# Optimization experiments

Hardware: AMD Instinct MI355X
Metric: run time of the kernel (lower is better)

Reference implementation:

```python
import jax, jax.numpy as jnp
import numpy as np

WS = 7        # window_size
HEADS = 8     # n_heads
SHIFT = WS // 2  # roll amount when shifted=True


def setup_inputs() -> dict:
    key = jax.random.key(0)
    k1, k2, k3 = jax.random.split(key, 3)
    B, C, H, W = 4, 256, 224, 224
    x = jax.random.normal(k1, (B, C, H, W), dtype=jnp.float32)
    # 1x1 conv weight [3C, C] (kernel dims squeezed) and bias [3C]
    w_qkv = jax.random.normal(k2, (3 * C, C), dtype=jnp.float32) * (1.0 / np.sqrt(C))
    b_qkv = jax.random.normal(k3, (3 * C,), dtype=jnp.float32) * 0.02
    return {"x": x, "w_qkv": w_qkv, "b_qkv": b_qkv}


def reference(x, w_qkv, b_qkv):
    B, C, H, W = x.shape
    hd = C // HEADS                      # head dim
    Hn, Wn = H // WS, W // WS            # windows per side

    # shifted: roll spatial dims by -window_size//2
    xs = jnp.roll(x, (-SHIFT, -SHIFT), axis=(-2, -1))

    # 1x1 conv: [B,C,H,W] -> [B,3C,H,W]
    qkv = jnp.einsum('bchw,oc->bohw', xs, w_qkv) + b_qkv[None, :, None, None]

    # window partition: [B,3C,H,W] -> (3, B, Hn, Wn, heads, ws*ws, hd)
    w = qkv.reshape(B, 3, HEADS, hd, Hn, WS, Wn, WS)
    w = jnp.transpose(w, (1, 0, 4, 6, 2, 5, 7, 3))  # 3,B,Hn,Wn,heads,ws,ws,hd
    w = w.reshape(3, B, Hn, Wn, HEADS, WS * WS, hd)
    q, k, v = w[0], w[1], w[2]

    # per-window SDPA (torch default scale = 1/sqrt(head_dim), no mask)
    scale = 1.0 / np.sqrt(hd)
    scores = jnp.einsum('bxyhqd,bxyhkd->bxyhqk', q, k) * scale
    attn = jax.nn.softmax(scores, axis=-1)
    out = jnp.einsum('bxyhqk,bxyhkd->bxyhqd', attn, v)  # B,Hn,Wn,heads,ws2,hd

    # window merge: back to [B,C,H,W]
    out = out.reshape(B, Hn, Wn, HEADS, WS, WS, hd)
    out = jnp.transpose(out, (0, 3, 6, 1, 4, 2, 5))  # B,heads,hd,Hn,ws,Wn,ws
    out = out.reshape(B, C, H, W)

    # inverse roll
    out = jnp.roll(out, (SHIFT, SHIFT), axis=(-2, -1))
    return out
```

## Files before the change

### kernel.cpp

```cpp
#include <hip/hip_runtime.h>

typedef __attribute__((ext_vector_type(8))) __bf16 bf16x8;
typedef __attribute__((ext_vector_type(4))) __bf16 bf16x4;
typedef __attribute__((ext_vector_type(4))) float f32x4;

#define MFMA16(a, b, c) __builtin_amdgcn_mfma_f32_16x16x32_bf16(a, b, c, 0, 0, 0)

#define BAR() asm volatile("s_waitcnt lgkmcnt(0)\n\ts_barrier" ::: "memory")

constexpr int HH = 224, WW = 224, CC = 256;
constexpr int HW = HH * WW;
constexpr int SH = 3;
constexpr int NTOK = 49;

constexpr int QS = 40;
constexpr int VTS = 68;
constexpr int PS = 72;
constexpr int XSS = 264;
constexpr int SZ_QK = 2 * NTOK * QS;
constexpr int OFF_VT = SZ_QK;
constexpr int SZ_VT = 32 * VTS;
constexpr int XS_OFF = OFF_VT + SZ_VT;
constexpr int SMEM_SZ = XS_OFF + NTOK * XSS;

__global__ void __launch_bounds__(256) cvt_w(const float* __restrict__ w,
                                             __bf16* __restrict__ o) {
  int i = blockIdx.x * 256 + threadIdx.x;
  int e = i & 7;
  int l15 = (i >> 3) & 15;
  int quad = (i >> 7) & 3;
  int ks = (i >> 9) & 7;
  int g = i >> 12;
  int h = g / 6, nip = g - h * 6;
  int row = (nip >> 1) * 256 + h * 32 + (nip & 1) * 16 + l15;
  int col = ks * 32 + quad * 8 + e;
  o[i] = (__bf16)w[row * 256 + col];
}

__global__ void __launch_bounds__(256, 4)
swin_attn(const float* __restrict__ x, const __bf16* __restrict__ wbf,
          const float* __restrict__ bias, float* __restrict__ out) {
  __shared__ __bf16 sm[SMEM_SZ];

  const int tid = threadIdx.x;
  const int lane = tid & 63;
  const int wave = tid >> 6;
  const int quad = lane >> 4;
  const int l15 = lane & 15;
  const int wa = wave >> 1, wb = wave & 1;

  int blk = blockIdx.x;
  int win = (blk & 7) * 512 + (blk >> 3);
  int b = win >> 10;
  int hn = (win >> 5) & 31;
  int wn = win & 31;
  int r0 = hn * 7, c0 = wn * 7;

  for (int idx = tid; idx < NTOK * CC; idx += 256) {
    int c = idx / NTOK;
    int p = idx - c * NTOK;
    int pi = p / 7, pj = p - pi * 7;
    int gr = r0 + pi + SH; if (gr >= HH) gr -= HH;
    int gc = c0 + pj + SH; if (gc >= WW) gc -= WW;
    sm[XS_OFF + p * XSS + c] = (__bf16)x[((b * CC + c) * HH + gr) * WW + gc];
  }

  int stok = wave * 16 + l15;
  bool svalid = stok < NTOK;
  int spix;
  {
    int t = svalid ? stok : 48;
    int pi = t / 7, pj = t - pi * 7;
    int gr = r0 + pi + SH; if (gr >= HH) gr -= HH;
    int gc = c0 + pj + SH; if (gc >= WW) gc -= WW;
    spix = gr * WW + gc;
  }

  __bf16* qq = sm;
  __bf16* kk = sm + NTOK * QS;
  __bf16* vT = sm + OFF_VT;
  __bf16* P = sm;
  const float scale = 0.17677669529663687f;
  const f32x4 zero = {0.f, 0.f, 0.f, 0.f};

  const __bf16* wlane = wbf + quad * 128 + l15 * 8;

  for (int h = 0; h < 8; h++) {
    BAR();

    float bs[3];
    f32x4 acc[2][3];
#pragma unroll
    for (int i = 0; i < 3; i++) {
      int nip = 3 * wb + i;
      int o = (nip >> 1) * 256 + h * 32 + (nip & 1) * 16 + l15;
      bs[i] = bias[o];
      acc[0][i] = zero;
      acc[1][i] = zero;
    }
    const __bf16* wp = wlane + (h * 6 + 3 * wb) * 4096;

    bf16x8 wfr[4][3];
#pragma unroll
    for (int pk = 0; pk < 4; pk++)
#pragma unroll
      for (int i = 0; i < 3; i++)
        wfr[pk][i] = *(const bf16x8*)(wp + i * 4096 + pk * 512);

#pragma unroll
    for (int ks = 0; ks < 8; ks++) {
      bf16x8 bfr[3], afr[2];
#pragma unroll
      for (int i = 0; i < 3; i++) bfr[i] = wfr[ks & 3][i];
      if (ks < 4) {
#pragma unroll
        for (int i = 0; i < 3; i++)
          wfr[ks & 3][i] = *(const bf16x8*)(wp + i * 4096 + (ks + 4) * 512);
      }
#pragma unroll
      for (int mil = 0; mil < 2; mil++) {
        int m = (2 * wa + mil) * 16 + l15; if (m > 48) m = 48;
        afr[mil] = *(const bf16x8*)(sm + XS_OFF + m * XSS + ks * 32 + quad * 8);
      }
#pragma unroll
      for (int mil = 0; mil < 2; mil++)
#pragma unroll
        for (int i = 0; i < 3; i++)
          acc[mil][i] = MFMA16(afr[mil], bfr[i], acc[mil][i]);
    }
#pragma unroll
    for (int i = 0; i < 3; i++) {
      int nip = 3 * wb + i;
      int typ = nip >> 1;
      int dl = (nip & 1) * 16 + l15;
#pragma unroll
      for (int mil = 0; mil < 2; mil++) {
        int mi = 2 * wa + mil;
        if (typ == 2) {
          bf16x4 pk;
#pragma unroll
          for (int r = 0; r < 4; r++) {
            int tok = mi * 16 + quad * 4 + r;
            float v = acc[mil][i][r] + bs[i];
            pk[r] = (tok < NTOK) ? (__bf16)v : (__bf16)0.f;
          }
          *(bf16x4*)(vT + dl * VTS + mi * 16 + quad * 4) = pk;
        } else {
          __bf16* tgt = typ ? kk : qq;
#pragma unroll
          for (int r = 0; r < 4; r++) {
            int tok = mi * 16 + quad * 4 + r;
            if (tok < NTOK) tgt[tok * QS + dl] = (__bf16)(acc[mil][i][r] + bs[i]);
          }
        }
      }
    }
    BAR();

    int mq = wave * 16 + l15; if (mq > 48) mq = 48;
    bf16x8 aq = *(const bf16x8*)(qq + mq * QS + quad * 8);
    f32x4 sc[4];
#pragma unroll
    for (int ni = 0; ni < 4; ni++) {
      int n = ni * 16 + l15; if (n > 48) n = 48;
      bf16x8 bk = *(const bf16x8*)(kk + n * QS + quad * 8);
      sc[ni] = MFMA16(aq, bk, zero);
    }
    BAR();

#pragma unroll
    for (int r = 0; r < 4; r++) {
      float e[4];
      float sum = 0.f;
#pragma unroll
      for (int ni = 0; ni < 4; ni++) {
        float s = (ni * 16 + l15 < NTOK) ? sc[ni][r] * scale : -1e30f;
        float ev = __expf(s);
        e[ni] = ev;
        sum += ev;
      }
#pragma unroll
      for (int off = 1; off < 16; off <<= 1) sum += __shfl_xor(sum, off, 64);
      float inv = 1.f / sum;
      int row = wave * 16 + quad * 4 + r;
      if (row < NTOK) {
#pragma unroll
        for (int ni = 0; ni < 4; ni++)
          P[row * PS + ni * 16 + l15] = (__bf16)(e[ni] * inv);
      }
    }
    BAR();

    f32x4 oT[2] = {zero, zero};
    int prow = wave * 16 + l15; if (prow > 48) prow = 48;
#pragma unroll
    for (int ks = 0; ks < 2; ks++) {
      bf16x8 bp = *(const bf16x8*)(P + prow * PS + ks * 32 + quad * 8);
#pragma unroll
      for (int ni2 = 0; ni2 < 2; ni2++) {
        const __bf16* vp = vT + (ni2 * 16 + l15) * VTS + ks * 32 + quad * 8;
        bf16x4 lo = *(const bf16x4*)vp;
        bf16x4 hi = *(const bf16x4*)(vp + 4);
        bf16x8 av = __builtin_shufflevector(lo, hi, 0, 1, 2, 3, 4, 5, 6, 7);
        oT[ni2] = MFMA16(av, bp, oT[ni2]);
      }
    }

    int chbase = b * CC + h * 32;
    if (svalid) {
#pragma unroll
      for (int ni2 = 0; ni2 < 2; ni2++)
#pragma unroll
        for (int r = 0; r < 4; r++) {
          int ch = chbase + ni2 * 16 + quad * 4 + r;
          out[ch * HW + spix] = oT[ni2][r];
        }
    }
  }
}

extern "C" void kernel_launch(void* const* d_in, const int* in_sizes, int n_in,
                              void* d_out, int out_size, void* d_ws, size_t ws_size,
                              hipStream_t stream) {
  const float* x = (const float*)d_in[0];
  const float* w = (const float*)d_in[1];
  const float* bs = (const float*)d_in[2];
  float* out = (float*)d_out;
  __bf16* wbf = (__bf16*)d_ws;

  cvt_w<<<dim3(768), dim3(256), 0, stream>>>(w, wbf);
  swin_attn<<<dim3(4096), dim3(256), 0, stream>>>(x, wbf, bs, out);
}
```

Baseline: 549.2 us.

## Keep input fragments in registers and double-buffer per-head QKV in LDS

Each wave now loads its X A-fragments for all eight k-steps into registers once, instead of re-reading them from LDS for every head. The per-head Q/K/V^T tiles alternate between two LDS buffers, and the softmax P tile gets its own region, so two of the per-head barriers can be dropped and total LDS use shrinks. Weight fragments are now loaded inside each k-step rather than prefetched across steps. The cost is about 64 extra VGPRs per lane under a four-blocks-per-CU launch bound, which risks spills or lower occupancy, and global weight loads are less hidden.

Result: slower. 586.7 us (+6.8%).

```diff
diff --git a/kernel.cpp b/kernel.cpp
--- a/kernel.cpp
+++ b/kernel.cpp
@@ -17,11 +17,11 @@
 constexpr int VTS = 68;
 constexpr int PS = 72;
 constexpr int XSS = 264;
-constexpr int SZ_QK = 2 * NTOK * QS;
-constexpr int OFF_VT = SZ_QK;
-constexpr int SZ_VT = 32 * VTS;
-constexpr int XS_OFF = OFF_VT + SZ_VT;
-constexpr int SMEM_SZ = XS_OFF + NTOK * XSS;
+
+constexpr int P_OFF = 0;
+constexpr int BUF0 = 3528;
+constexpr int BUFSZ = 2 * NTOK * QS + 32 * VTS;
+constexpr int SMEM_SZ = BUF0 + 2 * BUFSZ;
 
 __global__ void __launch_bounds__(256) cvt_w(const float* __restrict__ w,
                                              __bf16* __restrict__ o) {
@@ -62,7 +62,7 @@
     int pi = p / 7, pj = p - pi * 7;
     int gr = r0 + pi + SH; if (gr >= HH) gr -= HH;
     int gc = c0 + pj + SH; if (gc >= WW) gc -= WW;
-    sm[XS_OFF + p * XSS + c] = (__bf16)x[((b * CC + c) * HH + gr) * WW + gc];
+    sm[p * XSS + c] = (__bf16)x[((b * CC + c) * HH + gr) * WW + gc];
   }
 
   int stok = wave * 16 + l15;
@@ -76,17 +76,31 @@
     spix = gr * WW + gc;
   }
 
-  __bf16* qq = sm;
-  __bf16* kk = sm + NTOK * QS;
-  __bf16* vT = sm + OFF_VT;
-  __bf16* P = sm;
+  BAR();
+
+  bf16x8 afr[2][8];
+#pragma unroll
+  for (int mil = 0; mil < 2; mil++) {
+    int m = (2 * wa + mil) * 16 + l15; if (m > 48) m = 48;
+    const __bf16* ap = sm + m * XSS + quad * 8;
+#pragma unroll
+    for (int ks = 0; ks < 8; ks++)
+      afr[mil][ks] = *(const bf16x8*)(ap + ks * 32);
+  }
+
+  BAR();
+
+  __bf16* P = sm + P_OFF;
   const float scale = 0.17677669529663687f;
   const f32x4 zero = {0.f, 0.f, 0.f, 0.f};
 
   const __bf16* wlane = wbf + quad * 128 + l15 * 8;
 
   for (int h = 0; h < 8; h++) {
-    BAR();
+    __bf16* buf = sm + BUF0 + (h & 1) * BUFSZ;
+    __bf16* qq = buf;
+    __bf16* kk = buf + NTOK * QS;
+    __bf16* vT = buf + 2 * NTOK * QS;
 
     float bs[3];
     f32x4 acc[2][3];
@@ -99,35 +113,19 @@
       acc[1][i] = zero;
     }
     const __bf16* wp = wlane + (h * 6 + 3 * wb) * 4096;
-
-    bf16x8 wfr[4][3];
-#pragma unroll
-    for (int pk = 0; pk < 4; pk++)
+#pragma unroll
+    for (int ks = 0; ks < 8; ks++) {
+      bf16x8 bfr[3];
 #pragma unroll
       for (int i = 0; i < 3; i++)
-        wfr[pk][i] = *(const bf16x8*)(wp + i * 4096 + pk * 512);
-
-#pragma unroll
-    for (int ks = 0; ks < 8; ks++) {
-      bf16x8 bfr[3], afr[2];
-#pragma unroll
-      for (int i = 0; i < 3; i++) bfr[i] = wfr[ks & 3][i];
-      if (ks < 4) {
+        bfr[i] = *(const bf16x8*)(wp + i * 4096 + ks * 512);
+#pragma unroll
+      for (int mil = 0; mil < 2; mil++)
 #pragma unroll
         for (int i = 0; i < 3; i++)
-          wfr[ks & 3][i] = *(const bf16x8*)(wp + i * 4096 + (ks + 4) * 512);
-      }
-#pragma unroll
-      for (int mil = 0; mil < 2; mil++) {
-        int m = (2 * wa + mil) * 16 + l15; if (m > 48) m = 48;
-        afr[mil] = *(const bf16x8*)(sm + XS_OFF + m * XSS + ks * 32 + quad * 8);
-      }
-#pragma unroll
-      for (int mil = 0; mil < 2; mil++)
-#pragma unroll
-        for (int i = 0; i < 3; i++)
-          acc[mil][i] = MFMA16(afr[mil], bfr[i], acc[mil][i]);
-    }
+          acc[mil][i] = MFMA16(afr[mil][ks], bfr[i], acc[mil][i]);
+    }
+
 #pragma unroll
     for (int i = 0; i < 3; i++) {
       int nip = 3 * wb + i;
@@ -155,6 +153,7 @@
         }
       }
     }
+
     BAR();
 
     int mq = wave * 16 + l15; if (mq > 48) mq = 48;
@@ -166,7 +165,6 @@
       bf16x8 bk = *(const bf16x8*)(kk + n * QS + quad * 8);
       sc[ni] = MFMA16(aq, bk, zero);
     }
-    BAR();
 
 #pragma unroll
     for (int r = 0; r < 4; r++) {
@@ -189,7 +187,7 @@
           P[row * PS + ni * 16 + l15] = (__bf16)(e[ni] * inv);
       }
     }
-    BAR();
+
 
     f32x4 oT[2] = {zero, zero};
     int prow = wave * 16 + l15; if (prow > 48) prow = 48;
```
